# Kernel tuning notes

Measured on AMD Instinct MI355X. Metric: run time of the kernel, lower is better.

## Reference

```python
import jax, jax.numpy as jnp
import numpy as np

NC, NPR, E, B = 200000, 100000, 500000, 200000
DIN, HID, HEADS = 16, 256, 8
D = HID // HEADS
NCOLOR, NSIZE, NGROUP = 1000, 30, 50


def setup_inputs() -> dict:
    key = jax.random.key(0)
    ks = jax.random.split(key, 24)
    g = lambda i, shape, s=0.05: jax.random.normal(ks[i], shape, jnp.float32) * s
    return dict(
        customer_x=g(0, (NC, DIN), 1.0),
        product_x=g(1, (NPR, DIN), 1.0),
        proj_cust_W=g(2, (DIN, HID)), proj_cust_b=jnp.zeros((HID,), jnp.float32),
        proj_prod_W=g(3, (DIN, HID)), proj_prod_b=jnp.zeros((HID,), jnp.float32),
        att_src_r=g(4, (HEADS, D)), att_dst_r=g(5, (HEADS, D)),
        att_src_rb=g(6, (HEADS, D)), att_dst_rb=g(7, (HEADS, D)),
        q_sem=g(8, (HID,)), k_lin_W=g(9, (HID, HID)), k_lin_b=jnp.zeros((HID,), jnp.float32),
        color_emb=g(10, (NCOLOR, 8), 1.0),
        size_emb=g(11, (NSIZE, 4), 1.0),
        group_emb=g(12, (NGROUP, 4), 1.0),
        fc1_W=g(13, (HID * 2 + 16, 128)), fc1_b=jnp.zeros((128,), jnp.float32),
        fc2_W=g(14, (128, 32)), fc2_b=jnp.zeros((32,), jnp.float32),
        fc3_W=g(15, (32, 1)), fc3_b=jnp.zeros((1,), jnp.float32),
        bn1_gamma=jnp.ones((128,), jnp.float32), bn1_beta=jnp.zeros((128,), jnp.float32),
        bn2_gamma=jnp.ones((32,), jnp.float32), bn2_beta=jnp.zeros((32,), jnp.float32),
        edge_src=jax.random.randint(ks[16], (E,), 0, NC),
        edge_dst=jax.random.randint(ks[17], (E,), 0, NPR),
        label_src=jax.random.randint(ks[18], (B,), 0, NC),
        label_dst=jax.random.randint(ks[19], (B,), 0, NPR),
        size_idx=jax.random.randint(ks[20], (B,), 0, NSIZE),
        color_idx=jax.random.randint(ks[21], (B,), 0, NCOLOR),
        group_idx=jax.random.randint(ks[22], (B,), 0, NGROUP),
    )


def _edge_softmax(logits, dst, n):
    # destination-grouped softmax over edges; logits: [E,H]
    m = jax.ops.segment_max(logits, dst, num_segments=n)
    m = jnp.where(jnp.isfinite(m), m, 0.0)
    e = jnp.exp(logits - m[dst])
    s = jax.ops.segment_sum(e, dst, num_segments=n)
    return e / (s[dst] + 1e-16)


def _han_relation(h_src, h_dst, a_src, a_dst, src, dst, n_dst):
    # h_*: [N,H,D]; a_*: [H,D]
    logits = (h_src * a_src).sum(-1)[src] + (h_dst * a_dst).sum(-1)[dst]  # [E,H]
    logits = jax.nn.leaky_relu(logits, 0.2)
    alpha = _edge_softmax(logits, dst, n_dst)
    msg = alpha[:, :, None] * h_src[src]  # [E,H,D]
    out = jax.ops.segment_sum(msg, dst, num_segments=n_dst)
    return jax.nn.relu(out.reshape(n_dst, -1))  # [N_dst, H*D]


def _group(outs, q, kW, kb):
    # semantic attention over metapaths (PyG HANConv group)
    stk = jnp.stack(outs)  # [M,N,F]
    score = (q * jnp.tanh(stk @ kW + kb).mean(1)).sum(-1)  # [M]
    attn = jax.nn.softmax(score)
    return jnp.einsum('m,mnf->nf', attn, stk)


def _bn(x, gamma, beta):
    mu = x.mean(0)
    var = x.var(0)
    return (x - mu) * jax.lax.rsqrt(var + 1e-5) * gamma + beta


def reference(customer_x, product_x, proj_cust_W, proj_cust_b, proj_prod_W, proj_prod_b,
              att_src_r, att_dst_r, att_src_rb, att_dst_rb, q_sem, k_lin_W, k_lin_b,
              color_emb, size_emb, group_emb, fc1_W, fc1_b, fc2_W, fc2_b, fc3_W, fc3_b,
              bn1_gamma, bn1_beta, bn2_gamma, bn2_beta,
              edge_src, edge_dst, label_src, label_dst, size_idx, color_idx, group_idx):
    h_c = (customer_x @ proj_cust_W + proj_cust_b).reshape(-1, HEADS, D)
    h_p = (product_x @ proj_prod_W + proj_prod_b).reshape(-1, HEADS, D)
    # relation customer -returns-> product
    out_p = _han_relation(h_c, h_p, att_src_r, att_dst_r, edge_src, edge_dst, NPR)
    # relation product -returned_by-> customer (reversed edges)
    out_c = _han_relation(h_p, h_c, att_src_rb, att_dst_rb, edge_dst, edge_src, NC)
    cust = _group([out_c], q_sem, k_lin_W, k_lin_b)  # [NC, 256]
    prod = _group([out_p], q_sem, k_lin_W, k_lin_b)  # [NPR, 256]
    feat = jnp.concatenate([cust[label_src], prod[label_dst],
                            size_emb[size_idx], color_emb[color_idx], group_emb[group_idx]], axis=-1)
    x = jax.nn.relu(feat @ fc1_W + fc1_b)
    x = _bn(x, bn1_gamma, bn1_beta)
    x = jax.nn.relu(x @ fc2_W + fc2_b)
    x = _bn(x, bn2_gamma, bn2_beta)
    return x @ fc3_W + fc3_b
```

## Files before the change

### kernel.cpp

```cpp
#include <hip/hip_runtime.h>

#define NCC 200000
#define NPRR 100000
#define NEE 500000
#define NBB 200000

typedef __attribute__((ext_vector_type(8))) short bf16x8;
typedef __attribute__((ext_vector_type(16))) float f32x16;

__device__ __forceinline__ float b2f(unsigned short u){ return __uint_as_float(((unsigned)u)<<16); }
__device__ __forceinline__ unsigned short f2b(float f){
  unsigned x = __float_as_uint(f);
  return (unsigned short)((x + 0x7fffu + ((x>>16)&1u)) >> 16);
}

__global__ __launch_bounds__(256) void wa_prep2(
    const float* __restrict__ Wc, const float* __restrict__ bc,
    const float* __restrict__ attAc, const float* __restrict__ attBc,
    const float* __restrict__ Wp, const float* __restrict__ bp,
    const float* __restrict__ attAp, const float* __restrict__ attBp,
    float* __restrict__ WAc, float* __restrict__ WAp)
{
  int tid = threadIdx.x;
  for (int task = tid; task < 4*17*8; task += 256) {
    int grp = task / 136, rem = task % 136;
    int k = rem >> 3, h = rem & 7;
    const float* att = (grp==0)?attAc:(grp==1)?attBc:(grp==2)?attAp:attBp;
    const float* W   = (grp<2)?Wc:Wp;
    const float* bias= (grp<2)?bc:bp;
    const float* row = (k < 16) ? (W + k*256) : bias;
    float acc = 0.f;
    for (int d = 0; d < 32; d++) acc = fmaf(row[h*32+d], att[h*32+d], acc);
    if (grp<2) WAc[(grp&1)*136 + rem] = acc;
    else       WAp[(grp&1)*136 + rem] = acc;
  }
}

__global__ __launch_bounds__(256) void prep_proj(
    const float* __restrict__ Wc, const float* __restrict__ Wp,
    const float* __restrict__ WAc, const float* __restrict__ WAp,
    unsigned short* __restrict__ WtC, unsigned short* __restrict__ WtP,
    unsigned short* __restrict__ WAtC, unsigned short* __restrict__ WAtP)
{
  int idx = blockIdx.x*256 + threadIdx.x;
  if (idx < 4096){ int n=idx>>4, k=idx&15; WtC[idx]=f2b(Wc[k*256+n]); }
  else if (idx < 8192){ int t=idx-4096; int n=t>>4, k=t&15; WtP[t]=f2b(Wp[k*256+n]); }
  else if (idx < 8704){ int t=idx-8192; int n=t>>4, k=t&15;
    WAtC[t] = (n<16)? f2b(WAc[(n>>3)*136 + k*8 + (n&7)]) : (unsigned short)0; }
  else if (idx < 9216){ int t=idx-8704; int n=t>>4, k=t&15;
    WAtP[t] = (n<16)? f2b(WAp[(n>>3)*136 + k*8 + (n&7)]) : (unsigned short)0; }
}

__global__ __launch_bounds__(256) void prep_fc1(const float* __restrict__ fc1W,
    const float* __restrict__ fc1b,
    const float* __restrict__ size_emb, const float* __restrict__ color_emb,
    const float* __restrict__ group_emb,
    unsigned short* __restrict__ BtC, unsigned short* __restrict__ BtP,
    float* __restrict__ Ts, float* __restrict__ Tc, float* __restrict__ Tg)
{
  int idx = blockIdx.x*256 + threadIdx.x;
  if (idx < 32768){
    int n = idx>>8, k = idx&255;
    BtC[idx] = f2b(fc1W[k*128 + n]);
  } else if (idx < 65536){
    int t = idx - 32768;
    int n = t>>8, k = t&255;
    BtP[t] = f2b(fc1W[(256+k)*128 + n]);
  } else if (idx < 65536 + 30*128){
    int t = idx - 65536;
    int s = t>>7, j = t&127;
    float a = fc1b[j];
    #pragma unroll
    for (int c=0;c<4;c++) a = fmaf(size_emb[s*4+c], fc1W[(512+c)*128+j], a);
    Ts[t] = a;
  } else if (idx < 65536 + 30*128 + 1000*128){
    int t = idx - 65536 - 30*128;
    int col = t>>7, j = t&127;
    float a = 0.f;
    #pragma unroll
    for (int c=0;c<8;c++) a = fmaf(color_emb[col*8+c], fc1W[(516+c)*128+j], a);
    Tc[t] = a;
  } else if (idx < 65536 + 30*128 + 1000*128 + 50*128){
    int t = idx - 65536 - 30*128 - 1000*128;
    int g = t>>7, j = t&127;
    float a = 0.f;
    #pragma unroll
    for (int c=0;c<4;c++) a = fmaf(group_emb[g*4+c], fc1W[(524+c)*128+j], a);
    Tg[t] = a;
  }
}

__global__ __launch_bounds__(256) void proj_mfma(const float* __restrict__ X,
    const unsigned short* __restrict__ Wt, const unsigned short* __restrict__ WAt,
    const float* __restrict__ WA,
    unsigned short* __restrict__ H, float* __restrict__ sA, float* __restrict__ sB,
    int N, int nt)
{
  __shared__ unsigned short wt[4608];
  __shared__ float biasS[16];
  int tid = threadIdx.x;
  for (int i=tid; i<512; i+=256) ((uint4*)wt)[i] = ((const uint4*)Wt)[i];
  for (int i=tid; i<64;  i+=256) ((uint4*)(wt+4096))[i] = ((const uint4*)WAt)[i];
  if (tid < 16) biasS[tid] = WA[(tid>>3)*136 + 128 + (tid&7)];
  __syncthreads();
  int wv = tid>>6, lane = tid&63, m = lane&31, hi = lane>>5;
  for (int t = blockIdx.x; t < nt; t += gridDim.x){
    int node = t*32 + m;
    bf16x8 a;
    {
      const float4* xr = (const float4*)(X + (long long)node*16 + hi*8);
      float4 f0 = xr[0], f1 = xr[1];
      unsigned short av[8] = {f2b(f0.x),f2b(f0.y),f2b(f0.z),f2b(f0.w),
                              f2b(f1.x),f2b(f1.y),f2b(f1.z),f2b(f1.w)};
      a = *(bf16x8*)av;
    }
    #pragma unroll
    for (int s=0;s<2;s++){
      int c0 = wv*64 + s*32;
      bf16x8 b = *(const bf16x8*)(wt + (c0+m)*16 + hi*8);
      f32x16 acc;
      #pragma unroll
      for (int i=0;i<16;i++) acc[i]=0.f;
      acc = __builtin_amdgcn_mfma_f32_32x32x16_bf16(a, b, acc, 0, 0, 0);
      #pragma unroll
      for (int reg=0; reg<16; reg++){
        int row = (reg&3) + 8*(reg>>2) + 4*hi;
        H[(long long)(t*32+row)*256 + c0 + m] = f2b(acc[reg]);
      }
    }
    if (wv == 0){
      bf16x8 b = *(const bf16x8*)(wt + 4096 + m*16 + hi*8);
      f32x16 acc;
      #pragma unroll
      for (int i=0;i<16;i++) acc[i]=0.f;
      acc = __builtin_amdgcn_mfma_f32_32x32x16_bf16(a, b, acc, 0, 0, 0);
      if (m < 16){
        float bias = biasS[m];
        float* dst = (m < 8) ? sA : sB;
        int h = m & 7;
        #pragma unroll
        for (int reg=0; reg<16; reg++){
          int row = (reg&3) + 8*(reg>>2) + 4*hi;
          dst[(long long)(t*32+row)*8 + h] = acc[reg] + bias;
        }
      }
    }
  }
}

__global__ __launch_bounds__(256) void hist2u(const int* __restrict__ src, const int* __restrict__ dst,
    int* __restrict__ cnt_c, int* __restrict__ cnt_p, int E,
    const int* __restrict__ lsrc, const int* __restrict__ ldst,
    int* __restrict__ used_c, int* __restrict__ used_p, int B)
{
  int e = blockIdx.x*256 + threadIdx.x;
  if (e < E){
    atomicAdd(&cnt_p[dst[e]], 1);
    atomicAdd(&cnt_c[src[e]], 1);
  }
  if (e < B){
    used_c[lsrc[e]] = 1;
    used_p[ldst[e]] = 1;
  }
}

__global__ __launch_bounds__(256) void scan_p1f(const int* __restrict__ cnt_p, int* __restrict__ bsum_p, int Np,
    const int* __restrict__ cnt_c, int* __restrict__ bsum_c, int Nc, int BP)
{
  __shared__ int red[256];
  const int* cnt; int* bsum; int N; int blk;
  if ((int)blockIdx.x < BP){ cnt=cnt_p; bsum=bsum_p; N=Np; blk=blockIdx.x; }
  else                     { cnt=cnt_c; bsum=bsum_c; N=Nc; blk=blockIdx.x-BP; }
  int tid = threadIdx.x;
  int base = blk*1024 + tid*4;
  int s = 0;
  #pragma unroll
  for (int k=0;k<4;k++){ int i=base+k; if (i<N) s += cnt[i]; }
  red[tid] = s;
  __syncthreads();
  for (int off=128; off>0; off>>=1){ if (tid<off) red[tid]+=red[tid+off]; __syncthreads(); }
  if (tid==0) bsum[blk] = red[0];
}

__global__ __launch_bounds__(256) void scan_p2f(int* __restrict__ bsum_p, int Bp, int* __restrict__ rowptr_p, int Np,
    int* __restrict__ bsum_c, int Bc, int* __restrict__ rowptr_c, int Nc)
{
  __shared__ int ts[256];
  int* bsum; int B; int* rowptr; int N;
  if (blockIdx.x == 0){ bsum=bsum_p; B=Bp; rowptr=rowptr_p; N=Np; }
  else                { bsum=bsum_c; B=Bc; rowptr=rowptr_c; N=Nc; }
  int tid = threadIdx.x;
  int v = (tid<B) ? bsum[tid] : 0;
  ts[tid] = v;
  __syncthreads();
  for (int off=1; off<256; off<<=1){
    int t = (tid>=off) ? ts[tid-off] : 0;
    __syncthreads();
    ts[tid] += t;
    __syncthreads();
  }
  if (tid < B) bsum[tid] = ts[tid] - v;
  if (tid == B-1) rowptr[N] = ts[tid];
}

__global__ __launch_bounds__(256) void scan_p3f(const int* __restrict__ cnt_p, const int* __restrict__ bsum_p,
    int* __restrict__ rowptr_p, int Np,
    const int* __restrict__ cnt_c, const int* __restrict__ bsum_c,
    int* __restrict__ rowptr_c, int Nc, int BP)
{
  __shared__ int ts[256];
  const int* cnt; const int* bsum; int* rowptr; int N; int blk;
  if ((int)blockIdx.x < BP){ cnt=cnt_p; bsum=bsum_p; rowptr=rowptr_p; N=Np; blk=blockIdx.x; }
  else                     { cnt=cnt_c; bsum=bsum_c; rowptr=rowptr_c; N=Nc; blk=blockIdx.x-BP; }
  int tid = threadIdx.x;
  int base = blk*1024 + tid*4;
  int v[4]; int s = 0;
  #pragma unroll
  for (int k=0;k<4;k++){ int i=base+k; v[k] = (i<N) ? cnt[i] : 0; s += v[k]; }
  ts[tid] = s;
  __syncthreads();
  for (int off=1; off<256; off<<=1){
    int t = (tid>=off) ? ts[tid-off] : 0;
    __syncthreads();
    ts[tid] += t;
    __syncthreads();
  }
  int run = bsum[blk] + ts[tid] - s;
  #pragma unroll
  for (int k=0;k<4;k++){ int i=base+k; if (i<N){ rowptr[i]=run; run += v[k]; } }
}

__global__ __launch_bounds__(256) void place2(const int* __restrict__ src, const int* __restrict__ dst,
    const int* __restrict__ rp_r, const int* __restrict__ rp_rb,
    int* __restrict__ cnt_p, int* __restrict__ cnt_c,
    int* __restrict__ si_r, int* __restrict__ si_rb, int E)
{
  int e = blockIdx.x*256 + threadIdx.x;
  if (e >= E) return;
  int s = src[e], d = dst[e];
  si_r [rp_r [d] + atomicAdd(&cnt_p[d], 1)] = s;
  si_rb[rp_rb[s] + atomicAdd(&cnt_c[s], 1)] = d;
}

__global__ __launch_bounds__(256) void agg_gemm(
    const int* __restrict__ rowptr, const int* __restrict__ srcidx,
    const float* __restrict__ sSrc, const float* __restrict__ sDst,
    const unsigned short* __restrict__ H, const unsigned short* __restrict__ Bt,
    unsigned short* __restrict__ Y, const int* __restrict__ used)
{
  __shared__ unsigned short feat[32*264];
  int tid = threadIdx.x;
  int wv = tid>>6, lane = tid&63;
  int g = lane>>4, ln = lane&15, h = ln>>2;
  h = (lane&15) >> 1;
  long long base = (long long)blockIdx.x*32;
  #pragma unroll
  for (int t=0;t<2;t++){
    int r = wv*8 + t*4 + g;
    long long n = base + r;
    float acc[16];
    #pragma unroll
    for (int c=0;c<16;c++) acc[c]=0.f;
    float den = 0.f;
    if (used[n]){
      int e0 = rowptr[n], e1 = rowptr[n+1];
      int elast = e1 - 1;
      float sdh = sDst[n*8 + h];
      for (int e = e0; e < e1; e += 4){
        int i1 = min(e+1, elast), i2 = min(e+2, elast), i3 = min(e+3, elast);
        int s0 = srcidx[e],  s1 = srcidx[i1];
        int s2 = srcidx[i2], s3 = srcidx[i3];
        const uint4* p0 = (const uint4*)&H[(long long)s0*256 + ln*16];
        const uint4* p1 = (const uint4*)&H[(long long)s1*256 + ln*16];
        const uint4* p2 = (const uint4*)&H[(long long)s2*256 + ln*16];
        const uint4* p3 = (const uint4*)&H[(long long)s3*256 + ln*16];
        uint4 uA0 = p0[0], uA1 = p0[1];
        uint4 uB0 = p1[0], uB1 = p1[1];
        uint4 uC0 = p2[0], uC1 = p2[1];
        uint4 uD0 = p3[0], uD1 = p3[1];
        float l0 = sSrc[(long long)s0*8 + h];
        float l1 = sSrc[(long long)s1*8 + h];
        float l2 = sSrc[(long long)s2*8 + h];
        float l3 = sSrc[(long long)s3*8 + h];
        l0 += sdh; l1 += sdh; l2 += sdh; l3 += sdh;
        float w0 = __expf(l0 > 0.f ? l0 : 0.2f*l0);
        float w1 = (e+1 < e1) ? __expf(l1 > 0.f ? l1 : 0.2f*l1) : 0.f;
        float w2 = (e+2 < e1) ? __expf(l2 > 0.f ? l2 : 0.2f*l2) : 0.f;
        float w3 = (e+3 < e1) ? __expf(l3 > 0.f ? l3 : 0.2f*l3) : 0.f;
        den += (w0 + w1) + (w2 + w3);
        unsigned ua[8] = {uA0.x,uA0.y,uA0.z,uA0.w, uA1.x,uA1.y,uA1.z,uA1.w};
        unsigned ub[8] = {uB0.x,uB0.y,uB0.z,uB0.w, uB1.x,uB1.y,uB1.z,uB1.w};
        unsigned uc[8] = {uC0.x,uC0.y,uC0.z,uC0.w, uC1.x,uC1.y,uC1.z,uC1.w};
        unsigned ud[8] = {uD0.x,uD0.y,uD0.z,uD0.w, uD1.x,uD1.y,uD1.z,uD1.w};
        #pragma unroll
        for (int p=0;p<8;p++){
          acc[p*2]   = fmaf(w0, b2f((unsigned short)(ua[p]&0xffffu)), acc[p*2]);
          acc[p*2+1] = fmaf(w0, b2f((unsigned short)(ua[p]>>16)),     acc[p*2+1]);
          acc[p*2]   = fmaf(w1, b2f((unsigned short)(ub[p]&0xffffu)), acc[p*2]);
          acc[p*2+1] = fmaf(w1, b2f((unsigned short)(ub[p]>>16)),     acc[p*2+1]);
          acc[p*2]   = fmaf(w2, b2f((unsigned short)(uc[p]&0xffffu)), acc[p*2]);
          acc[p*2+1] = fmaf(w2, b2f((unsigned short)(uc[p]>>16)),     acc[p*2+1]);
          acc[p*2]   = fmaf(w3, b2f((unsigned short)(ud[p]&0xffffu)), acc[p*2]);
          acc[p*2+1] = fmaf(w3, b2f((unsigned short)(ud[p]>>16)),     acc[p*2+1]);
        }
      }
    }
    float inv = 1.f/(den + 1e-16f);
    unsigned short ov[16];
    #pragma unroll
    for (int c=0;c<16;c++) ov[c] = f2b(fmaxf(acc[c]*inv, 0.f));
    *(uint4*)&feat[r*264 + ln*16]     = *(uint4*)&ov[0];
    *(uint4*)&feat[r*264 + ln*16 + 8] = *(uint4*)&ov[8];
  }
  __syncthreads();
  int m = lane&31, hi = lane>>5;
  f32x16 acc;
  #pragma unroll
  for (int i=0;i<16;i++) acc[i]=0.f;
  const unsigned short* ap  = feat + m*264 + hi*8;
  const unsigned short* btp = Bt + (wv*32 + m)*256 + hi*8;
  #pragma unroll 4
  for (int ks=0; ks<16; ks++){
    bf16x8 a = *(const bf16x8*)(ap + ks*16);
    bf16x8 b = *(const bf16x8*)(btp + ks*16);
    acc = __builtin_amdgcn_mfma_f32_32x32x16_bf16(a, b, acc, 0, 0, 0);
  }
  int col = wv*32 + m;
  #pragma unroll
  for (int reg=0; reg<16; reg++){
    int row = (reg&3) + 8*(reg>>2) + 4*hi;
    Y[(base+row)*128 + col] = f2b(acc[reg]);
  }
}

__global__ __launch_bounds__(256) void gather_fc1(
    const unsigned short* __restrict__ Yc, const unsigned short* __restrict__ Yp,
    const float* __restrict__ Ts, const float* __restrict__ Tc, const float* __restrict__ Tg,
    const int* __restrict__ lsrc, const int* __restrict__ ldst,
    const int* __restrict__ sidx, const int* __restrict__ cidx, const int* __restrict__ gidx,
    unsigned short* __restrict__ x1, float* __restrict__ bnsum, int ntiles)
{
  __shared__ float redS[16][128];
  __shared__ float redQ[16][128];
  int tid = threadIdx.x;
  int rl = tid>>4, g = tid&15;
  float sacc[8] = {0,0,0,0,0,0,0,0};
  float qacc[8] = {0,0,0,0,0,0,0,0};
  for (int t = blockIdx.x; t < ntiles; t += gridDim.x){
    long long row = (long long)t*16 + rl;
    int ls = lsrc[row], ld = ldst[row], si = sidx[row], ci = cidx[row], gi = gidx[row];
    uint4 uc = *(const uint4*)&Yc[(long long)ls*128 + g*8];
    uint4 up = *(const uint4*)&Yp[(long long)ld*128 + g*8];
    float4 t0 = *(const float4*)&Ts[si*128 + g*8];
    float4 t1 = *(const float4*)&Ts[si*128 + g*8 + 4];
    float4 c0 = *(const float4*)&Tc[ci*128 + g*8];
    float4 c1 = *(const float4*)&Tc[ci*128 + g*8 + 4];
    float4 g0 = *(const float4*)&Tg[gi*128 + g*8];
    float4 g1 = *(const float4*)&Tg[gi*128 + g*8 + 4];
    unsigned ucs[4] = {uc.x,uc.y,uc.z,uc.w};
    unsigned ups[4] = {up.x,up.y,up.z,up.w};
    float tb[8] = {t0.x+c0.x+g0.x, t0.y+c0.y+g0.y, t0.z+c0.z+g0.z, t0.w+c0.w+g0.w,
                   t1.x+c1.x+g1.x, t1.y+c1.y+g1.y, t1.z+c1.z+g1.z, t1.w+c1.w+g1.w};
    unsigned short ov[8];
    #pragma unroll
    for (int p=0;p<4;p++){
      float vl = b2f((unsigned short)(ucs[p]&0xffffu)) + b2f((unsigned short)(ups[p]&0xffffu)) + tb[p*2];
      float vh = b2f((unsigned short)(ucs[p]>>16))     + b2f((unsigned short)(ups[p]>>16))     + tb[p*2+1];
      vl = fmaxf(vl, 0.f); vh = fmaxf(vh, 0.f);
      ov[p*2] = f2b(vl); ov[p*2+1] = f2b(vh);
      sacc[p*2]   += vl; qacc[p*2]   += vl*vl;
      sacc[p*2+1] += vh; qacc[p*2+1] += vh*vh;
    }
    *(uint4*)&x1[row*128 + g*8] = *(uint4*)ov;
  }
  #pragma unroll
  for (int j=0;j<8;j++){ redS[rl][g*8+j]=sacc[j]; redQ[rl][g*8+j]=qacc[j]; }
  __syncthreads();
  if (tid < 128){
    float s=0.f, q=0.f;
    #pragma unroll
    for (int r=0;r<16;r++){ s += redS[r][tid]; q += redQ[r][tid]; }
    atomicAdd(&bnsum[tid], s);
    atomicAdd(&bnsum[128+tid], q);
  }
}

__global__ void bn1_fold(const float* __restrict__ bnsum,
    const float* __restrict__ gamma, const float* __restrict__ beta,
    const float* __restrict__ fc2W, const float* __restrict__ fc2b,
    unsigned short* __restrict__ Bt2, float* __restrict__ b2p, float invB)
{
  __shared__ float sc[128], sh[128];
  int tid = threadIdx.x;
  if (tid<128){
    float mu  = bnsum[tid]*invB;
    float var = bnsum[128+tid]*invB - mu*mu;
    float s = gamma[tid] * rsqrtf(var + 1e-5f);
    sc[tid]=s; sh[tid]= beta[tid] - mu*s;
  }
  __syncthreads();
  for (int idx=tid; idx<32*128; idx+=256){
    int n = idx>>7, k = idx&127;
    Bt2[idx] = f2b(sc[k]*fc2W[k*32+n]);
  }
  if (tid<32){
    float a = fc2b[tid];
    for (int k=0;k<128;k++) a = fmaf(sh[k], fc2W[k*32+tid], a);
    b2p[tid]=a;
  }
}

__global__ __launch_bounds__(256) void fc2_mfma(const unsigned short* __restrict__ x1,
    const unsigned short* __restrict__ Bt2, const float* __restrict__ b2p,
    unsigned short* __restrict__ x2, float* __restrict__ bnsum2, int M)
{
  __shared__ unsigned short xt[128*136];
  __shared__ unsigned short wt[32*136];
  __shared__ float redS[4][32];
  __shared__ float redQ[4][32];
  int tid = threadIdx.x;
  long long base = (long long)blockIdx.x*128;
  for (int idx=tid; idx<128*16; idx+=256){
    int r = idx>>4, c = idx&15;
    uint4 u = make_uint4(0,0,0,0);
    if (base + r < M) u = *(const uint4*)&x1[(base+r)*128 + c*8];
    *(uint4*)&xt[r*136 + c*8] = u;
  }
  for (int idx=tid; idx<32*16; idx+=256){
    int r = idx>>4, c = idx&15;
    *(uint4*)&wt[r*136 + c*8] = *(const uint4*)&Bt2[r*128 + c*8];
  }
  __syncthreads();
  int wv = tid>>6, lane = tid&63;
  int m = lane&31, hi = lane>>5;
  f32x16 acc;
  #pragma unroll
  for (int i=0;i<16;i++) acc[i]=0.f;
  const unsigned short* ap = xt + (wv*32 + m)*136 + hi*8;
  const unsigned short* bp = wt + m*136 + hi*8;
  #pragma unroll
  for (int ks=0; ks<8; ks++){
    bf16x8 a = *(const bf16x8*)(ap + ks*16);
    bf16x8 b = *(const bf16x8*)(bp + ks*16);
    acc = __builtin_amdgcn_mfma_f32_32x32x16_bf16(a, b, acc, 0, 0, 0);
  }
  int col = m;
  float bias = b2p[col];
  float s=0.f, q=0.f;
  #pragma unroll
  for (int reg=0; reg<16; reg++){
    int row = (reg&3) + 8*(reg>>2) + 4*hi;
    long long grow = base + wv*32 + row;
    float v = fmaxf(acc[reg] + bias, 0.f);
    if (grow < M) x2[grow*32 + col] = f2b(v);
    s += v; q += v*v;
  }
  if (base + 128 > M){
    s = 0.f; q = 0.f;
    #pragma unroll
    for (int reg=0; reg<16; reg++){
      int row = (reg&3) + 8*(reg>>2) + 4*hi;
      long long grow = base + wv*32 + row;
      float v = fmaxf(acc[reg] + bias, 0.f);
      if (grow < M){ s += v; q += v*v; }
    }
  }
  s += __shfl_xor(s, 32);
  q += __shfl_xor(q, 32);
  if (hi == 0){ redS[wv][col] = s; redQ[wv][col] = q; }
  __syncthreads();
  if (tid < 32){
    float a = redS[0][tid]+redS[1][tid]+redS[2][tid]+redS[3][tid];
    float b = redQ[0][tid]+redQ[1][tid]+redQ[2][tid]+redQ[3][tid];
    atomicAdd(&bnsum2[tid], a);
    atomicAdd(&bnsum2[32+tid], b);
  }
}

__global__ void bn2_fold(const float* __restrict__ bnsum2,
    const float* __restrict__ gamma2, const float* __restrict__ beta2,
    const float* __restrict__ fc3W, const float* __restrict__ fc3b,
    float* __restrict__ w3p, float invB)
{
  __shared__ float sh3[32];
  int tid = threadIdx.x;
  if (tid<32){
    float mu  = bnsum2[tid]*invB;
    float var = bnsum2[32+tid]*invB - mu*mu;
    float s   = gamma2[tid] * rsqrtf(var + 1e-5f);
    float shv = beta2[tid] - mu*s;
    float w   = fc3W[tid];
    w3p[tid]  = s*w;
    sh3[tid]  = shv*w;
  }
  __syncthreads();
  if (tid==0){
    float a = fc3b[0];
    for (int j=0;j<32;j++) a += sh3[j];
    w3p[32] = a;
  }
}

__global__ __launch_bounds__(256) void fc3_kernel(const unsigned short* __restrict__ x2,
    const float* __restrict__ w3p, float* __restrict__ out)
{
  __shared__ float wl[34];
  int tid = threadIdx.x;
  if (tid<33) wl[tid]=w3p[tid];
  __syncthreads();
  long long row = (long long)blockIdx.x*32 + (tid>>3);
  int j0 = (tid&7)*4;
  uint2 u = *(const uint2*)(x2 + row*32 + j0);
  float a = b2f((unsigned short)(u.x&0xffffu))*wl[j0]
          + b2f((unsigned short)(u.x>>16))   *wl[j0+1]
          + b2f((unsigned short)(u.y&0xffffu))*wl[j0+2]
          + b2f((unsigned short)(u.y>>16))   *wl[j0+3];
  a += __shfl_xor(a,1);
  a += __shfl_xor(a,2);
  a += __shfl_xor(a,4);
  if ((tid&7)==0) out[row] = a + wl[32];
}

extern "C" void kernel_launch(void* const* d_in, const int* in_sizes, int n_in,
                              void* d_out, int out_size, void* d_ws, size_t ws_size,
                              hipStream_t stream)
{
  (void)in_sizes; (void)n_in; (void)out_size; (void)ws_size;
  const float* customer_x = (const float*)d_in[0];
  const float* product_x  = (const float*)d_in[1];
  const float* pcW = (const float*)d_in[2];
  const float* pcB = (const float*)d_in[3];
  const float* ppW = (const float*)d_in[4];
  const float* ppB = (const float*)d_in[5];
  const float* att_src_r  = (const float*)d_in[6];
  const float* att_dst_r  = (const float*)d_in[7];
  const float* att_src_rb = (const float*)d_in[8];
  const float* att_dst_rb = (const float*)d_in[9];
  const float* color_emb = (const float*)d_in[13];
  const float* size_emb  = (const float*)d_in[14];
  const float* group_emb = (const float*)d_in[15];
  const float* fc1W = (const float*)d_in[16];
  const float* fc1b = (const float*)d_in[17];
  const float* fc2W = (const float*)d_in[18];
  const float* fc2b = (const float*)d_in[19];
  const float* fc3W = (const float*)d_in[20];
  const float* fc3b = (const float*)d_in[21];
  const float* bn1g = (const float*)d_in[22];
  const float* bn1b = (const float*)d_in[23];
  const float* bn2g = (const float*)d_in[24];
  const float* bn2b = (const float*)d_in[25];
  const int* edge_src  = (const int*)d_in[26];
  const int* edge_dst  = (const int*)d_in[27];
  const int* label_src = (const int*)d_in[28];
  const int* label_dst = (const int*)d_in[29];
  const int* size_idx  = (const int*)d_in[30];
  const int* color_idx = (const int*)d_in[31];
  const int* group_idx = (const int*)d_in[32];

  char* ws = (char*)d_ws;
  size_t off = 0;
  auto alloc = [&](size_t bytes)->char* {
    char* p = ws + off;
    off += (bytes + 255) & ~(size_t)255;
    return p;
  };
  unsigned short* H_c  = (unsigned short*)alloc((size_t)NCC*256*2);
  unsigned short* H_p  = (unsigned short*)alloc((size_t)NPRR*256*2);
  unsigned short* slab = (unsigned short*)alloc((size_t)NPRR*256*2);
  float* s_cr     = (float*)alloc((size_t)NCC*8*4);
  float* s_crb    = (float*)alloc((size_t)NCC*8*4);
  float* s_pr     = (float*)alloc((size_t)NPRR*8*4);
  float* s_prb    = (float*)alloc((size_t)NPRR*8*4);
  int* rowptr_r   = (int*)alloc((size_t)(NPRR+1)*4);
  int* rowptr_rb  = (int*)alloc((size_t)(NCC+1)*4);
  int* srcidx_r   = (int*)alloc((size_t)NEE*4);
  int* srcidx_rb  = (int*)alloc((size_t)NEE*4);
  int* cnts       = (int*)alloc((size_t)(NCC+NPRR)*3*4);
  int* cnt_c      = cnts;
  int* cnt_p      = cnts + NCC;
  int* cnt_c2     = cnts + NCC + NPRR;
  int* cnt_p2     = cnts + NCC + NPRR + NCC;
  int* used_c     = cnts + (NCC + NPRR)*2;
  int* used_p     = used_c + NCC;
  int* bsum_c     = (int*)alloc(256*4);
  int* bsum_p     = (int*)alloc(256*4);
  unsigned short* BtC = (unsigned short*)alloc(128*256*2);
  unsigned short* BtP = (unsigned short*)alloc(128*256*2);
  float* Ts     = (float*)alloc(30*128*4);
  float* Tc     = (float*)alloc(1000*128*4);
  float* Tg     = (float*)alloc(50*128*4);
  float* wa_c   = (float*)alloc(272*4);
  float* wa_p   = (float*)alloc(272*4);
  unsigned short* WtC  = (unsigned short*)alloc(256*16*2);
  unsigned short* WtP  = (unsigned short*)alloc(256*16*2);
  unsigned short* WAtC = (unsigned short*)alloc(32*16*2);
  unsigned short* WAtP = (unsigned short*)alloc(32*16*2);
  float* bnsum1 = (float*)alloc(256*4);
  float* bnsum2 = (float*)alloc(64*4);
  unsigned short* Bt2 = (unsigned short*)alloc(32*128*2);
  float* b2p    = (float*)alloc(32*4);
  float* w3p    = (float*)alloc(34*4);
  unsigned short* Y_p = slab;
  unsigned short* Y_c = H_c;
  unsigned short* x1b = H_p;
  unsigned short* x2b = (unsigned short*)s_cr;

  hipMemsetAsync(bnsum1, 0, 1280, stream);
  hipMemsetAsync(cnts, 0, (size_t)(NCC+NPRR)*3*4, stream);

  wa_prep2<<<1,256,0,stream>>>(pcW, pcB, att_src_r, att_dst_rb,
                               ppW, ppB, att_dst_r, att_src_rb, wa_c, wa_p);
  prep_proj<<<36,256,0,stream>>>(pcW, ppW, wa_c, wa_p, WtC, WtP, WAtC, WAtP);
  prep_fc1<<<(203776+255)/256,256,0,stream>>>(fc1W, fc1b, size_emb, color_emb, group_emb,
      BtC, BtP, Ts, Tc, Tg);

  proj_mfma<<<2048,256,0,stream>>>(customer_x, WtC, WAtC, wa_c, H_c, s_cr, s_crb, NCC, NCC/32);
  proj_mfma<<<2048,256,0,stream>>>(product_x,  WtP, WAtP, wa_p, H_p, s_pr, s_prb, NPRR, NPRR/32);

  const int eg = (NEE+255)/256;
  const int BP = (NPRR+1023)/1024;
  const int BC = (NCC +1023)/1024;
  hist2u<<<eg,256,0,stream>>>(edge_src, edge_dst, cnt_c, cnt_p, NEE,
      label_src, label_dst, used_c, used_p, NBB);
  scan_p1f<<<BP+BC,256,0,stream>>>(cnt_p, bsum_p, NPRR, cnt_c, bsum_c, NCC, BP);
  scan_p2f<<<2,256,0,stream>>>(bsum_p, BP, rowptr_r, NPRR, bsum_c, BC, rowptr_rb, NCC);
  scan_p3f<<<BP+BC,256,0,stream>>>(cnt_p, bsum_p, rowptr_r, NPRR,
      cnt_c, bsum_c, rowptr_rb, NCC, BP);
  place2<<<eg,256,0,stream>>>(edge_src, edge_dst, rowptr_r, rowptr_rb,
      cnt_p2, cnt_c2, srcidx_r, srcidx_rb, NEE);

  agg_gemm<<<NPRR/32,256,0,stream>>>(rowptr_r,  srcidx_r,  s_cr,  s_pr,  H_c, BtP, Y_p, used_p);
  agg_gemm<<<NCC/32,256,0,stream>>>(rowptr_rb, srcidx_rb, s_prb, s_crb, H_p, BtC, Y_c, used_c);

  gather_fc1<<<2048,256,0,stream>>>(Y_c, Y_p, Ts, Tc, Tg,
      label_src, label_dst, size_idx, color_idx, group_idx, x1b, bnsum1, NBB/16);

  bn1_fold<<<1,256,0,stream>>>(bnsum1, bn1g, bn1b, fc2W, fc2b, Bt2, b2p, 1.0f/NBB);
  fc2_mfma<<<(NBB+127)/128,256,0,stream>>>(x1b, Bt2, b2p, x2b, bnsum2, NBB);
  bn2_fold<<<1,64,0,stream>>>(bnsum2, bn2g, bn2b, fc3W, fc3b, w3p, 1.0f/NBB);
  fc3_kernel<<<NBB/32,256,0,stream>>>(x2b, w3p, (float*)d_out);
}
```

Measured before the change: 575.9 us.

## Compact used destination nodes into a work list before aggregation GEMM

```diff
diff --git a/kernel.cpp b/kernel.cpp
--- a/kernel.cpp
+++ b/kernel.cpp
@@ -242,30 +242,55 @@
   si_rb[rp_rb[s] + atomicAdd(&cnt_c[s], 1)] = d;
 }
 
+__global__ __launch_bounds__(256) void compact2(
+    const int* __restrict__ used_p, const int* __restrict__ rowptr_p, int Np,
+    int4* __restrict__ list_p, int* __restrict__ lcnt_p,
+    const int* __restrict__ used_c, const int* __restrict__ rowptr_c, int Nc,
+    int4* __restrict__ list_c, int* __restrict__ lcnt_c)
+{
+  int n = blockIdx.x*256 + threadIdx.x;
+  if (n < Np && used_p[n]){
+    int slot = atomicAdd(lcnt_p, 1);
+    list_p[slot] = make_int4(n, rowptr_p[n], rowptr_p[n+1], 0);
+  }
+  if (n < Nc && used_c[n]){
+    int slot = atomicAdd(lcnt_c, 1);
+    list_c[slot] = make_int4(n, rowptr_c[n], rowptr_c[n+1], 0);
+  }
+}
+
 __global__ __launch_bounds__(256) void agg_gemm(
-    const int* __restrict__ rowptr, const int* __restrict__ srcidx,
+    const int4* __restrict__ list, const int* __restrict__ lcnt,
+    const int* __restrict__ srcidx,
     const float* __restrict__ sSrc, const float* __restrict__ sDst,
     const unsigned short* __restrict__ H, const unsigned short* __restrict__ Bt,
-    unsigned short* __restrict__ Y, const int* __restrict__ used)
+    unsigned short* __restrict__ Y)
 {
   __shared__ unsigned short feat[32*264];
+  __shared__ int nid[32];
+  int cnt = *lcnt;
+  int base = blockIdx.x*32;
+  if (base >= cnt) return;
   int tid = threadIdx.x;
   int wv = tid>>6, lane = tid&63;
-  int g = lane>>4, ln = lane&15, h = ln>>2;
-  h = (lane&15) >> 1;
-  long long base = (long long)blockIdx.x*32;
+  int g = lane>>4, ln = lane&15, h = ln>>1;
   #pragma unroll
   for (int t=0;t<2;t++){
     int r = wv*8 + t*4 + g;
-    long long n = base + r;
+    int slot = base + r;
     float acc[16];
     #pragma unroll
     for (int c=0;c<16;c++) acc[c]=0.f;
     float den = 0.f;
-    if (used[n]){
-      int e0 = rowptr[n], e1 = rowptr[n+1];
+    int node = -1, e0 = 0, e1 = 0;
+    if (slot < cnt){
+      int4 L = list[slot];
+      node = L.x; e0 = L.y; e1 = L.z;
+    }
+    if (ln == 0) nid[r] = node;
+    if (node >= 0 && e1 > e0){
       int elast = e1 - 1;
-      float sdh = sDst[n*8 + h];
+      float sdh = sDst[(long long)node*8 + h];
       for (int e = e0; e < e1; e += 4){
         int i1 = min(e+1, elast), i2 = min(e+2, elast), i3 = min(e+3, elast);
         int s0 = srcidx[e],  s1 = srcidx[i1];
@@ -329,7 +354,8 @@
   #pragma unroll
   for (int reg=0; reg<16; reg++){
     int row = (reg&3) + 8*(reg>>2) + 4*hi;
-    Y[(base+row)*128 + col] = f2b(acc[reg]);
+    int nd = nid[row];
+    if (nd >= 0) Y[(long long)nd*128 + col] = f2b(acc[reg]);
   }
 }
 
@@ -584,6 +610,9 @@
   int* used_p     = used_c + NCC;
   int* bsum_c     = (int*)alloc(256*4);
   int* bsum_p     = (int*)alloc(256*4);
+  int4* list_p    = (int4*)alloc((size_t)NPRR*16);
+  int4* list_c    = (int4*)alloc((size_t)NCC*16);
+  int* lcnt       = (int*)alloc(256);
   unsigned short* BtC = (unsigned short*)alloc(128*256*2);
   unsigned short* BtP = (unsigned short*)alloc(128*256*2);
   float* Ts     = (float*)alloc(30*128*4);
@@ -607,6 +636,7 @@
 
   hipMemsetAsync(bnsum1, 0, 1280, stream);
   hipMemsetAsync(cnts, 0, (size_t)(NCC+NPRR)*3*4, stream);
+  hipMemsetAsync(lcnt, 0, 256, stream);
 
   wa_prep2<<<1,256,0,stream>>>(pcW, pcB, att_src_r, att_dst_rb,
                                ppW, ppB, att_dst_r, att_src_rb, wa_c, wa_p);
@@ -628,9 +658,11 @@
       cnt_c, bsum_c, rowptr_rb, NCC, BP);
   place2<<<eg,256,0,stream>>>(edge_src, edge_dst, rowptr_r, rowptr_rb,
       cnt_p2, cnt_c2, srcidx_r, srcidx_rb, NEE);
-
-  agg_gemm<<<NPRR/32,256,0,stream>>>(rowptr_r,  srcidx_r,  s_cr,  s_pr,  H_c, BtP, Y_p, used_p);
-  agg_gemm<<<NCC/32,256,0,stream>>>(rowptr_rb, srcidx_rb, s_prb, s_crb, H_p, BtC, Y_c, used_c);
+  compact2<<<(NCC+255)/256,256,0,stream>>>(used_p, rowptr_r, NPRR, list_p, &lcnt[0],
+      used_c, rowptr_rb, NCC, list_c, &lcnt[1]);
+
+  agg_gemm<<<NPRR/32,256,0,stream>>>(list_p, &lcnt[0], srcidx_r,  s_cr,  s_pr,  H_c, BtP, Y_p);
+  agg_gemm<<<NCC/32,256,0,stream>>>(list_c, &lcnt[1], srcidx_rb, s_prb, s_crb, H_p, BtC, Y_c);
 
   gather_fc1<<<2048,256,0,stream>>>(Y_c, Y_p, Ts, Tc, Tg,
       label_src, label_dst, size_idx, color_idx, group_idx, x1b, bnsum1, NBB/16);
```

New measurement: 603.3 us. 4.8% more time.
